# Optimization experiments

Hardware: AMD Instinct MI355X
Metric: run time of the kernel (lower is better)

Reference implementation:

```python
import jax, jax.numpy as jnp
import numpy as np

E = 1024
H = 16
EPS = 1e-5


def setup_inputs() -> dict:
    key = jax.random.key(0)
    ks = jax.random.split(key, 17)
    B, T = 8, 1024
    s = 0.02
    inp = {
        'x': jax.random.normal(ks[0], (B, T, E), dtype=jnp.float32),
        'Wq': jax.random.normal(ks[1], (E, E), dtype=jnp.float32) * s,
        'bq': jnp.zeros((E,), jnp.float32),
        'Wk': jax.random.normal(ks[2], (E, E), dtype=jnp.float32) * s,
        'bk': jnp.zeros((E,), jnp.float32),
        'Wv': jax.random.normal(ks[3], (E, E), dtype=jnp.float32) * s,
        'bv': jnp.zeros((E,), jnp.float32),
        'Wo': jax.random.normal(ks[4], (E, E), dtype=jnp.float32) * s,
        'bo': jnp.zeros((E,), jnp.float32),
        'W1': jax.random.normal(ks[5], (E, 4 * E), dtype=jnp.float32) * s,
        'b1': jnp.zeros((4 * E,), jnp.float32),
        'W2': jax.random.normal(ks[6], (4 * E, E), dtype=jnp.float32) * s,
        'b2': jnp.zeros((E,), jnp.float32),
        'g1': jnp.ones((E,), jnp.float32),
        'be1': jnp.zeros((E,), jnp.float32),
        'g2': jnp.ones((E,), jnp.float32),
        'be2': jnp.zeros((E,), jnp.float32),
    }
    return inp


def _layernorm(x, g, b):
    mu = jnp.mean(x, axis=-1, keepdims=True)
    var = jnp.mean(jnp.square(x - mu), axis=-1, keepdims=True)
    return (x - mu) * jax.lax.rsqrt(var + EPS) * g + b


def _block(x, Wq, bq, Wk, bk, Wv, bv, Wo, bo, W1, b1, W2, b2, g1, be1, g2, be2):
    B, T, Ee = x.shape
    hd = Ee // H
    q = (x @ Wq + bq).reshape(B, T, H, hd).transpose(0, 2, 1, 3)  # (B,H,T,d)
    k = (x @ Wk + bk).reshape(B, T, H, hd).transpose(0, 2, 1, 3)
    v = (x @ Wv + bv).reshape(B, T, H, hd).transpose(0, 2, 1, 3)
    scores = jnp.einsum('bhqd,bhkd->bhqk', q, k) / jnp.sqrt(jnp.float32(hd))
    causal = jnp.tril(jnp.ones((T, T), bool))
    scores = jnp.where(causal, scores, -jnp.inf)
    w = jax.nn.softmax(scores, axis=-1)
    attn = jnp.einsum('bhqk,bhkd->bhqd', w, v)
    attn = attn.transpose(0, 2, 1, 3).reshape(B, T, Ee)
    attn = attn @ Wo + bo  # dropout is identity (p=0 / eval)
    x = _layernorm(x + attn, g1, be1)
    ff = jax.nn.relu(x @ W1 + b1) @ W2 + b2
    x = _layernorm(x + ff, g2, be2)
    return x


def reference(x, Wq, bq, Wk, bk, Wv, bv, Wo, bo, W1, b1, W2, b2, g1, be1, g2, be2):
    return _block(x, Wq, bq, Wk, bk, Wv, bv, Wo, bo, W1, b1, W2, b2, g1, be1, g2, be2)
```

## Files before the change

### kernel.cpp

```cpp
#include <hip/hip_runtime.h>
#include <math.h>

typedef unsigned short u16;
typedef __attribute__((ext_vector_type(8))) short short8;
typedef __attribute__((ext_vector_type(4))) float floatx4;

__device__ __forceinline__ u16 f2bf(float f) {
    unsigned u = __float_as_uint(f);
    unsigned r = u + 0x7fffu + ((u >> 16) & 1u);
    return (u16)(r >> 16);
}

__device__ __forceinline__ void gload16(const u16* g, u16* l) {
    __builtin_amdgcn_global_load_lds((const __attribute__((address_space(1))) void*)g,
                                     (__attribute__((address_space(3))) void*)l, 16, 0, 0);
}

template<int EPI>
__global__ __launch_bounds__(256) void gemm_mfma(
    const u16* __restrict__ A, const u16* __restrict__ Bt,
    const float* __restrict__ bias, const float* __restrict__ bias2,
    const float* __restrict__ bias3, const float* __restrict__ R,
    void* __restrict__ Cout, void* __restrict__ out2, void* __restrict__ out3,
    int M, int N, int K) {
    __shared__ u16 As[128 * 32];
    __shared__ u16 Bs[128 * 32];
    const int tid = threadIdx.x;
    const int wave = tid >> 6, lane = tid & 63;
    const int lrow = lane & 15, quad = lane >> 4;
    const int ny = M >> 7;
    const int by = blockIdx.x % ny, bx = blockIdx.x / ny;
    const int m0 = by * 128, n0 = bx * 128;
    const int wm = (wave & 1) * 64, wn = (wave >> 1) * 64;

    floatx4 acc[4][4];
#pragma unroll
    for (int i = 0; i < 4; i++)
#pragma unroll
        for (int j = 0; j < 4; j++) acc[i][j] = {0.f, 0.f, 0.f, 0.f};

    const int f0 = wave * 128 + lane;

    for (int k0 = 0; k0 < K; k0 += 32) {
        __syncthreads();
#pragma unroll
        for (int i = 0; i < 2; i++) {
            int f = f0 + i * 64;
            int row = f >> 2, c = f & 3;
            int cg = c ^ ((row >> 1) & 3);
            gload16(A + (size_t)(m0 + row) * K + k0 + cg * 8, As + f * 8);
            gload16(Bt + (size_t)(n0 + row) * K + k0 + cg * 8, Bs + f * 8);
        }
        __syncthreads();
        short8 af[4], bf[4];
#pragma unroll
        for (int mt = 0; mt < 4; mt++) {
            int row = wm + mt * 16 + lrow;
            int ch = quad ^ ((lrow >> 1) & 3);
            af[mt] = *(const short8*)(As + row * 32 + ch * 8);
        }
#pragma unroll
        for (int nt = 0; nt < 4; nt++) {
            int row = wn + nt * 16 + lrow;
            int ch = quad ^ ((lrow >> 1) & 3);
            bf[nt] = *(const short8*)(Bs + row * 32 + ch * 8);
        }
#pragma unroll
        for (int mt = 0; mt < 4; mt++)
#pragma unroll
            for (int nt = 0; nt < 4; nt++)
                acc[mt][nt] = __builtin_amdgcn_mfma_f32_16x16x32_bf16(af[mt], bf[nt], acc[mt][nt], 0, 0, 0);
    }

    const float* bp = bias;
    int sec = 0;
    if (EPI == 4) {
        sec = n0 >> 10;
        bp = sec == 0 ? bias : (sec == 1 ? bias2 : bias3);
    }
    float bv[4];
#pragma unroll
    for (int nt = 0; nt < 4; nt++) {
        int gc = n0 + wn + nt * 16 + lrow;
        bv[nt] = bp[EPI == 4 ? (gc & 1023) : gc];
    }

#pragma unroll
    for (int mt = 0; mt < 4; mt++) {
        int gr0 = m0 + wm + mt * 16 + quad * 4;
#pragma unroll
        for (int nt = 0; nt < 4; nt++) {
            int gc = n0 + wn + nt * 16 + lrow;
            floatx4 a = acc[mt][nt];
            if (EPI == 1) {
                u16* C = (u16*)Cout;
#pragma unroll
                for (int r = 0; r < 4; r++)
                    C[(size_t)(gr0 + r) * N + gc] = f2bf(fmaxf(a[r] + bv[nt], 0.f));
            } else if (EPI == 2) {
                float* C = (float*)Cout;
#pragma unroll
                for (int r = 0; r < 4; r++) {
                    size_t idx = (size_t)(gr0 + r) * N + gc;
                    C[idx] = a[r] + bv[nt] + R[idx];
                }
            } else {
                int nc = gc & 1023;
                if (sec < 2) {
                    u16* C = (u16*)(sec == 0 ? Cout : out2);
#pragma unroll
                    for (int r = 0; r < 4; r++)
                        C[(size_t)(gr0 + r) * 1024 + nc] = f2bf(a[r] + bv[nt]);
                } else {
                    u16* C = (u16*)out3;
                    int bb = gr0 >> 10, t0 = gr0 & 1023;
                    size_t idx = ((size_t)(bb * 1024 + nc)) * 1024 + t0;
                    ushort4 u;
                    u.x = f2bf(a[0] + bv[nt]); u.y = f2bf(a[1] + bv[nt]);
                    u.z = f2bf(a[2] + bv[nt]); u.w = f2bf(a[3] + bv[nt]);
                    *(ushort4*)(C + idx) = u;
                }
            }
        }
    }
}

__global__ __launch_bounds__(256) void attn_mfma(
    const u16* __restrict__ q, const u16* __restrict__ k,
    const u16* __restrict__ vT, u16* __restrict__ o) {
    __shared__ u16 Kb[2][64 * 64];
    __shared__ u16 Vb[2][64 * 64];
    __shared__ u16 Pb[4][2][16 * 72];

    const int tid = threadIdx.x;
    const int wave = tid >> 6, lane = tid & 63;
    const int lrow = lane & 15, quad = lane >> 4;
    const int qb = blockIdx.y, bh = blockIdx.x;
    const int b = bh >> 4, h = bh & 15;
    const size_t tokbase = (size_t)b * 1024;
    const int ktmax = qb * 2 + 1;

#pragma unroll
    for (int i = 0; i < 2; i++) {
        int f = wave * 128 + i * 64 + lane;
        int row = f >> 3, c = f & 7, cg = c ^ (row & 7);
        gload16(q + (tokbase + qb * 128 + row) * 1024 + h * 64 + cg * 8, Kb[1] + f * 8);
        gload16(q + (tokbase + qb * 128 + 64 + row) * 1024 + h * 64 + cg * 8, Vb[1] + f * 8);
        gload16(k + (tokbase + row) * 1024 + h * 64 + cg * 8, Kb[0] + f * 8);
        gload16(vT + (tokbase + h * 64 + row) * 1024 + cg * 8, Vb[0] + f * 8);
    }
    asm volatile("s_waitcnt vmcnt(0)" ::: "memory");
    __syncthreads();
    short8 aQ[2][2];
#pragma unroll
    for (int band = 0; band < 2; band++)
#pragma unroll
        for (int ks = 0; ks < 2; ks++) {
            int row = wave * 16 + lrow;
            int pos = (ks * 4 + quad) ^ (lrow & 7);
            const u16* src = band ? Vb[1] : Kb[1];
            aQ[band][ks] = *(const short8*)(src + row * 64 + pos * 8);
        }
    __syncthreads();

    float lp[2][4];
    floatx4 oa[2][4];
#pragma unroll
    for (int bd = 0; bd < 2; bd++)
#pragma unroll
        for (int i = 0; i < 4; i++) { lp[bd][i] = 0.f; oa[bd][i] = {0.f, 0.f, 0.f, 0.f}; }

    for (int kt = 0; kt <= ktmax; kt++) {
        const int cur = kt & 1;
        if (kt < ktmax) {
            const int nxt = cur ^ 1;
#pragma unroll
            for (int i = 0; i < 2; i++) {
                int f = wave * 128 + i * 64 + lane;
                int row = f >> 3, c = f & 7, cg = c ^ (row & 7);
                gload16(k + (tokbase + (kt + 1) * 64 + row) * 1024 + h * 64 + cg * 8, Kb[nxt] + f * 8);
                gload16(vT + (tokbase + h * 64 + row) * 1024 + (kt + 1) * 64 + cg * 8, Vb[nxt] + f * 8);
            }
        }
#pragma unroll
        for (int band = 0; band < 2; band++) {
            const int btile = qb * 2 + band;
            if (kt > btile) continue;
            floatx4 sacc[4];
#pragma unroll
            for (int nt = 0; nt < 4; nt++) sacc[nt] = {0.f, 0.f, 0.f, 0.f};
#pragma unroll
            for (int nt = 0; nt < 4; nt++)
#pragma unroll
                for (int ks = 0; ks < 2; ks++) {
                    int row = nt * 16 + lrow;
                    int pos = (ks * 4 + quad) ^ (lrow & 7);
                    short8 bK = *(const short8*)(Kb[cur] + row * 64 + pos * 8);
                    sacc[nt] = __builtin_amdgcn_mfma_f32_16x16x32_bf16(aQ[band][ks], bK, sacc[nt], 0, 0, 0);
                }
            const bool diag = (kt == btile);
            float p[4][4];
#pragma unroll
            for (int r = 0; r < 4; r++) {
                int qrl = wave * 16 + quad * 4 + r;
#pragma unroll
                for (int nt = 0; nt < 4; nt++) {
                    float e = exp2f(sacc[nt][r] * 0.18033688011112042f);
                    if (diag && (nt * 16 + lrow) > qrl) e = 0.f;
                    p[nt][r] = e;
                    lp[band][r] += e;
                }
            }
            u16* Pw = Pb[wave][band];
#pragma unroll
            for (int nt = 0; nt < 4; nt++)
#pragma unroll
                for (int r = 0; r < 4; r++) {
                    int row = quad * 4 + r, key = nt * 16 + lrow;
                    int pos = ((key >> 3) ^ (row & 7)) * 8 + (key & 7);
                    Pw[row * 72 + pos] = f2bf(p[nt][r]);
                }
            asm volatile("s_waitcnt lgkmcnt(0)" ::: "memory");
            short8 aP[2];
#pragma unroll
            for (int ks = 0; ks < 2; ks++) {
                int pos = (ks * 4 + quad) ^ (lrow & 7);
                aP[ks] = *(const short8*)(Pw + lrow * 72 + pos * 8);
            }
#pragma unroll
            for (int nt = 0; nt < 4; nt++)
#pragma unroll
                for (int ks = 0; ks < 2; ks++) {
                    int row = nt * 16 + lrow;
                    int pos = (ks * 4 + quad) ^ (lrow & 7);
                    short8 bV = *(const short8*)(Vb[cur] + row * 64 + pos * 8);
                    oa[band][nt] = __builtin_amdgcn_mfma_f32_16x16x32_bf16(aP[ks], bV, oa[band][nt], 0, 0, 0);
                }
        }
        __syncthreads();
    }

#pragma unroll
    for (int band = 0; band < 2; band++) {
        float inv[4];
#pragma unroll
        for (int r = 0; r < 4; r++) {
            float l = lp[band][r];
#pragma unroll
            for (int off = 1; off < 16; off <<= 1) l += __shfl_xor(l, off);
            inv[r] = 1.f / l;
        }
#pragma unroll
        for (int nt = 0; nt < 4; nt++)
#pragma unroll
            for (int r = 0; r < 4; r++) {
                int grow = qb * 128 + band * 64 + wave * 16 + quad * 4 + r;
                float v = oa[band][nt][r] * inv[r];
                o[(tokbase + grow) * 1024 + h * 64 + nt * 16 + lrow] = f2bf(v);
            }
    }
}

__device__ __forceinline__ void tconv_tile(const float* __restrict__ W, u16* __restrict__ Wt,
                                           int K, int N, int k0, int n0, int t,
                                           float (*Ts)[33]) {
    const int r = t >> 3, c4 = (t & 7) * 4;
    float4 v = *(const float4*)(W + (size_t)(k0 + r) * N + n0 + c4);
    Ts[c4 + 0][r] = v.x; Ts[c4 + 1][r] = v.y; Ts[c4 + 2][r] = v.z; Ts[c4 + 3][r] = v.w;
    __syncthreads();
    ushort4 u;
    u.x = f2bf(Ts[r][c4 + 0]); u.y = f2bf(Ts[r][c4 + 1]);
    u.z = f2bf(Ts[r][c4 + 2]); u.w = f2bf(Ts[r][c4 + 3]);
    *(ushort4*)(Wt + (size_t)(n0 + r) * K + k0 + c4) = u;
}

__global__ __launch_bounds__(256) void prep_kernel(
    const float* __restrict__ x, const float* __restrict__ Wq, const float* __restrict__ Wk,
    const float* __restrict__ Wv, const float* __restrict__ Wo, const float* __restrict__ W1,
    const float* __restrict__ W2, u16* __restrict__ xb, u16* __restrict__ Wqkvt,
    u16* __restrict__ Wot, u16* __restrict__ W1t, u16* __restrict__ W2t) {
    __shared__ float Ts[32][33];
    const int blk = blockIdx.x, t = threadIdx.x;
    if (blk < 4096) {
        size_t i = ((size_t)blk * 256 + t) * 8;
        float4 a = *(const float4*)(x + i);
        float4 b = *(const float4*)(x + i + 4);
        ushort4 u0, u1;
        u0.x = f2bf(a.x); u0.y = f2bf(a.y); u0.z = f2bf(a.z); u0.w = f2bf(a.w);
        u1.x = f2bf(b.x); u1.y = f2bf(b.y); u1.z = f2bf(b.z); u1.w = f2bf(b.w);
        *(ushort4*)(xb + i) = u0;
        *(ushort4*)(xb + i + 4) = u1;
    } else if (blk < 8192) {
        int s = blk - 4096;
        int which = s >> 10, tt = s & 1023;
        int n0 = (tt & 31) * 32, k0 = (tt >> 5) * 32;
        const float* W = which == 0 ? Wq : which == 1 ? Wk : which == 2 ? Wv : Wo;
        u16* Wt = which == 3 ? Wot : Wqkvt + (size_t)which * 1024 * 1024;
        tconv_tile(W, Wt, 1024, 1024, k0, n0, t, Ts);
    } else if (blk < 12288) {
        int tt = blk - 8192;
        int n0 = (tt & 127) * 32, k0 = (tt >> 7) * 32;
        tconv_tile(W1, W1t, 1024, 4096, k0, n0, t, Ts);
    } else {
        int tt = blk - 12288;
        int n0 = (tt & 31) * 32, k0 = (tt >> 5) * 32;
        tconv_tile(W2, W2t, 4096, 1024, k0, n0, t, Ts);
    }
}

template<int WB>
__global__ __launch_bounds__(256) void ln_kernel(float* __restrict__ x, const float* __restrict__ g,
                                                 const float* __restrict__ bta, u16* __restrict__ xb) {
    __shared__ float red[8];
    const int tid = threadIdx.x;
    float* rowp = x + (size_t)blockIdx.x * 1024;
    float4 val = ((const float4*)rowp)[tid];

    float s = val.x + val.y + val.z + val.w;
#pragma unroll
    for (int off = 32; off; off >>= 1) s += __shfl_down(s, off);
    if ((tid & 63) == 0) red[tid >> 6] = s;
    __syncthreads();
    float mu = (red[0] + red[1] + red[2] + red[3]) * (1.f / 1024.f);

    float dx = val.x - mu, dy = val.y - mu, dz = val.z - mu, dw = val.w - mu;
    float sq = dx * dx + dy * dy + dz * dz + dw * dw;
#pragma unroll
    for (int off = 32; off; off >>= 1) sq += __shfl_down(sq, off);
    if ((tid & 63) == 0) red[4 + (tid >> 6)] = sq;
    __syncthreads();
    float var = (red[4] + red[5] + red[6] + red[7]) * (1.f / 1024.f);
    float rs = rsqrtf(var + 1e-5f);

    float4 gv = ((const float4*)g)[tid];
    float4 bv = ((const float4*)bta)[tid];
    float4 ov;
    ov.x = dx * rs * gv.x + bv.x;
    ov.y = dy * rs * gv.y + bv.y;
    ov.z = dz * rs * gv.z + bv.z;
    ov.w = dw * rs * gv.w + bv.w;
    ((float4*)rowp)[tid] = ov;
    if (WB) {
        u16* rb = xb + (size_t)blockIdx.x * 1024 + tid * 4;
        ushort4 u;
        u.x = f2bf(ov.x); u.y = f2bf(ov.y); u.z = f2bf(ov.z); u.w = f2bf(ov.w);
        *(ushort4*)rb = u;
    }
}

extern "C" void kernel_launch(void* const* d_in, const int* in_sizes, int n_in,
                              void* d_out, int out_size, void* d_ws, size_t ws_size,
                              hipStream_t stream) {
    const float* x   = (const float*)d_in[0];
    const float* Wq  = (const float*)d_in[1];
    const float* bq  = (const float*)d_in[2];
    const float* Wk  = (const float*)d_in[3];
    const float* bk  = (const float*)d_in[4];
    const float* Wv  = (const float*)d_in[5];
    const float* bv  = (const float*)d_in[6];
    const float* Wo  = (const float*)d_in[7];
    const float* bo  = (const float*)d_in[8];
    const float* W1  = (const float*)d_in[9];
    const float* b1  = (const float*)d_in[10];
    const float* W2  = (const float*)d_in[11];
    const float* b2  = (const float*)d_in[12];
    const float* g1  = (const float*)d_in[13];
    const float* be1 = (const float*)d_in[14];
    const float* g2  = (const float*)d_in[15];
    const float* be2 = (const float*)d_in[16];
    float* out = (float*)d_out;

    u16* w = (u16*)d_ws;
    const size_t SZ_ACT = (size_t)8192 * 1024;
    u16* xb    = w;                  w += SZ_ACT;
    u16* Wqkvt = w;                  w += (size_t)3 * 1024 * 1024;
    u16* Wot   = w;                  w += 1024 * 1024;
    u16* W1t   = w;                  w += (size_t)4096 * 1024;
    u16* W2t   = w;                  w += (size_t)1024 * 4096;
    u16* qb    = w;                  w += SZ_ACT;
    u16* kb    = w;                  w += SZ_ACT;
    u16* vTb   = w;                  w += SZ_ACT;
    u16* attb  = w;                  w += SZ_ACT;
    u16* hbuf  = qb;

    const int M = 8192;
    dim3 blk(256);

    prep_kernel<<<dim3(16384), blk, 0, stream>>>(x, Wq, Wk, Wv, Wo, W1, W2,
                                                 xb, Wqkvt, Wot, W1t, W2t);

    gemm_mfma<4><<<dim3(24 * 64), blk, 0, stream>>>(xb, Wqkvt, bq, bk, bv, nullptr,
                                                    qb, kb, vTb, M, 3072, 1024);
    attn_mfma<<<dim3(128, 8), blk, 0, stream>>>(qb, kb, vTb, attb);
    gemm_mfma<2><<<dim3(8 * 64), blk, 0, stream>>>(attb, Wot, bo, nullptr, nullptr, x,
                                                   out, nullptr, nullptr, M, 1024, 1024);
    ln_kernel<1><<<dim3(8192), blk, 0, stream>>>(out, g1, be1, xb);
    gemm_mfma<1><<<dim3(32 * 64), blk, 0, stream>>>(xb, W1t, b1, nullptr, nullptr, nullptr,
                                                    hbuf, nullptr, nullptr, M, 4096, 1024);
    gemm_mfma<2><<<dim3(8 * 64), blk, 0, stream>>>(hbuf, W2t, b2, nullptr, nullptr, out,
                                                   out, nullptr, nullptr, M, 1024, 4096);
    ln_kernel<0><<<dim3(8192), blk, 0, stream>>>(out, g2, be2, nullptr);
}
```

Before: 522.8 us.

## Use 32x32 MFMA tiles and split-K with atomics for the W2 GEMM

Switches the GEMM inner loop from 16x16x32 to 32x32x16 bf16 MFMA instructions, using a 2x2 grid of 32x32 accumulators per wave, which cuts LDS fragment reads per MFMA. Adds a split-K mode for the FFN down-projection (K=4096): it launches twice as many blocks, each covering half of K, and accumulates into the output with float atomics. The residual plus b2 bias is pre-written into the output by the first layernorm kernel so the atomics only add partial sums. This trades higher occupancy on the small-N GEMM for atomic traffic and a summation order that is no longer deterministic.

```diff
diff --git a/kernel.cpp b/kernel.cpp
--- a/kernel.cpp
+++ b/kernel.cpp
@@ -4,6 +4,7 @@
 typedef unsigned short u16;
 typedef __attribute__((ext_vector_type(8))) short short8;
 typedef __attribute__((ext_vector_type(4))) float floatx4;
+typedef __attribute__((ext_vector_type(16))) float floatx16;
 
 __device__ __forceinline__ u16 f2bf(float f) {
     unsigned u = __float_as_uint(f);
@@ -27,21 +28,28 @@
     __shared__ u16 Bs[128 * 32];
     const int tid = threadIdx.x;
     const int wave = tid >> 6, lane = tid & 63;
-    const int lrow = lane & 15, quad = lane >> 4;
-    const int ny = M >> 7;
-    const int by = blockIdx.x % ny, bx = blockIdx.x / ny;
+    const int ar = lane & 31, hl = lane >> 5;
+    const int ny = M >> 7, nx = N >> 7;
+    const int per = ny * nx;
+    const int chunk = blockIdx.x / per, rem = blockIdx.x % per;
+    const int nchunks = gridDim.x / per;
+    const int by = rem % ny, bx = rem / ny;
     const int m0 = by * 128, n0 = bx * 128;
     const int wm = (wave & 1) * 64, wn = (wave >> 1) * 64;
-
-    floatx4 acc[4][4];
-#pragma unroll
-    for (int i = 0; i < 4; i++)
-#pragma unroll
-        for (int j = 0; j < 4; j++) acc[i][j] = {0.f, 0.f, 0.f, 0.f};
+    const int klen = K / nchunks;
+    const int kstart = chunk * klen, kend = kstart + klen;
+
+    floatx16 acc[2][2];
+#pragma unroll
+    for (int i = 0; i < 2; i++)
+#pragma unroll
+        for (int j = 0; j < 2; j++)
+#pragma unroll
+            for (int r = 0; r < 16; r++) acc[i][j][r] = 0.f;
 
     const int f0 = wave * 128 + lane;
 
-    for (int k0 = 0; k0 < K; k0 += 32) {
+    for (int k0 = kstart; k0 < kend; k0 += 32) {
         __syncthreads();
 #pragma unroll
         for (int i = 0; i < 2; i++) {
@@ -52,24 +60,34 @@
             gload16(Bt + (size_t)(n0 + row) * K + k0 + cg * 8, Bs + f * 8);
         }
         __syncthreads();
-        short8 af[4], bf[4];
-#pragma unroll
-        for (int mt = 0; mt < 4; mt++) {
-            int row = wm + mt * 16 + lrow;
-            int ch = quad ^ ((lrow >> 1) & 3);
-            af[mt] = *(const short8*)(As + row * 32 + ch * 8);
-        }
-#pragma unroll
-        for (int nt = 0; nt < 4; nt++) {
-            int row = wn + nt * 16 + lrow;
-            int ch = quad ^ ((lrow >> 1) & 3);
-            bf[nt] = *(const short8*)(Bs + row * 32 + ch * 8);
-        }
-#pragma unroll
-        for (int mt = 0; mt < 4; mt++)
-#pragma unroll
-            for (int nt = 0; nt < 4; nt++)
-                acc[mt][nt] = __builtin_amdgcn_mfma_f32_16x16x32_bf16(af[mt], bf[nt], acc[mt][nt], 0, 0, 0);
+        short8 af[2][2], bf[2][2];
+#pragma unroll
+        for (int mt = 0; mt < 2; mt++) {
+            int row = wm + mt * 32 + ar;
+            int sw = (row >> 1) & 3;
+#pragma unroll
+            for (int s = 0; s < 2; s++) {
+                int ch = (s * 2 + hl) ^ sw;
+                af[mt][s] = *(const short8*)(As + row * 32 + ch * 8);
+            }
+        }
+#pragma unroll
+        for (int nt = 0; nt < 2; nt++) {
+            int row = wn + nt * 32 + ar;
+            int sw = (row >> 1) & 3;
+#pragma unroll
+            for (int s = 0; s < 2; s++) {
+                int ch = (s * 2 + hl) ^ sw;
+                bf[nt][s] = *(const short8*)(Bs + row * 32 + ch * 8);
+            }
+        }
+#pragma unroll
+        for (int s = 0; s < 2; s++)
+#pragma unroll
+            for (int mt = 0; mt < 2; mt++)
+#pragma unroll
+                for (int nt = 0; nt < 2; nt++)
+                    acc[mt][nt] = __builtin_amdgcn_mfma_f32_32x32x16_bf16(af[mt][s], bf[nt][s], acc[mt][nt], 0, 0, 0);
     }
 
     const float* bp = bias;
@@ -78,51 +96,60 @@
         sec = n0 >> 10;
         bp = sec == 0 ? bias : (sec == 1 ? bias2 : bias3);
     }
-    float bv[4];
-#pragma unroll
-    for (int nt = 0; nt < 4; nt++) {
-        int gc = n0 + wn + nt * 16 + lrow;
-        bv[nt] = bp[EPI == 4 ? (gc & 1023) : gc];
-    }
-
-#pragma unroll
-    for (int mt = 0; mt < 4; mt++) {
-        int gr0 = m0 + wm + mt * 16 + quad * 4;
-#pragma unroll
-        for (int nt = 0; nt < 4; nt++) {
-            int gc = n0 + wn + nt * 16 + lrow;
-            floatx4 a = acc[mt][nt];
-            if (EPI == 1) {
-                u16* C = (u16*)Cout;
-#pragma unroll
-                for (int r = 0; r < 4; r++)
-                    C[(size_t)(gr0 + r) * N + gc] = f2bf(fmaxf(a[r] + bv[nt], 0.f));
-            } else if (EPI == 2) {
-                float* C = (float*)Cout;
-#pragma unroll
-                for (int r = 0; r < 4; r++) {
-                    size_t idx = (size_t)(gr0 + r) * N + gc;
-                    C[idx] = a[r] + bv[nt] + R[idx];
+    float bv[2];
+    if (EPI != 5) {
+#pragma unroll
+        for (int nt = 0; nt < 2; nt++) {
+            int gc = n0 + wn + nt * 32 + ar;
+            bv[nt] = bp[EPI == 4 ? (gc & 1023) : gc];
+        }
+    }
+
+#pragma unroll
+    for (int mt = 0; mt < 2; mt++)
+#pragma unroll
+        for (int nt = 0; nt < 2; nt++) {
+            floatx16 a = acc[mt][nt];
+            int gc = n0 + wn + nt * 32 + ar;
+#pragma unroll
+            for (int rg = 0; rg < 4; rg++) {
+                int gr0 = m0 + wm + mt * 32 + rg * 8 + hl * 4;
+                if (EPI == 1) {
+                    u16* C = (u16*)Cout;
+#pragma unroll
+                    for (int rr = 0; rr < 4; rr++)
+                        C[(size_t)(gr0 + rr) * N + gc] = f2bf(fmaxf(a[rg * 4 + rr] + bv[nt], 0.f));
+                } else if (EPI == 2) {
+                    float* C = (float*)Cout;
+#pragma unroll
+                    for (int rr = 0; rr < 4; rr++) {
+                        size_t idx = (size_t)(gr0 + rr) * N + gc;
+                        C[idx] = a[rg * 4 + rr] + bv[nt] + R[idx];
+                    }
+                } else if (EPI == 5) {
+                    float* C = (float*)Cout;
+#pragma unroll
+                    for (int rr = 0; rr < 4; rr++)
+                        unsafeAtomicAdd(&C[(size_t)(gr0 + rr) * N + gc], a[rg * 4 + rr]);
+                } else {
+                    int nc = gc & 1023;
+                    if (sec < 2) {
+                        u16* C = (u16*)(sec == 0 ? Cout : out2);
+#pragma unroll
+                        for (int rr = 0; rr < 4; rr++)
+                            C[(size_t)(gr0 + rr) * 1024 + nc] = f2bf(a[rg * 4 + rr] + bv[nt]);
+                    } else {
+                        u16* C = (u16*)out3;
+                        int bb = gr0 >> 10, t0 = gr0 & 1023;
+                        size_t idx = ((size_t)(bb * 1024 + nc)) * 1024 + t0;
+                        ushort4 u;
+                        u.x = f2bf(a[rg * 4 + 0] + bv[nt]); u.y = f2bf(a[rg * 4 + 1] + bv[nt]);
+                        u.z = f2bf(a[rg * 4 + 2] + bv[nt]); u.w = f2bf(a[rg * 4 + 3] + bv[nt]);
+                        *(ushort4*)(C + idx) = u;
+                    }
                 }
-            } else {
-                int nc = gc & 1023;
-                if (sec < 2) {
-                    u16* C = (u16*)(sec == 0 ? Cout : out2);
-#pragma unroll
-                    for (int r = 0; r < 4; r++)
-                        C[(size_t)(gr0 + r) * 1024 + nc] = f2bf(a[r] + bv[nt]);
-                } else {
-                    u16* C = (u16*)out3;
-                    int bb = gr0 >> 10, t0 = gr0 & 1023;
-                    size_t idx = ((size_t)(bb * 1024 + nc)) * 1024 + t0;
-                    ushort4 u;
-                    u.x = f2bf(a[0] + bv[nt]); u.y = f2bf(a[1] + bv[nt]);
-                    u.z = f2bf(a[2] + bv[nt]); u.w = f2bf(a[3] + bv[nt]);
-                    *(ushort4*)(C + idx) = u;
-                }
-            }
-        }
-    }
+            }
+        }
 }
 
 __global__ __launch_bounds__(256) void attn_mfma(
@@ -308,9 +335,10 @@
     }
 }
 
-template<int WB>
+template<int WB, int ADDB>
 __global__ __launch_bounds__(256) void ln_kernel(float* __restrict__ x, const float* __restrict__ g,
-                                                 const float* __restrict__ bta, u16* __restrict__ xb) {
+                                                 const float* __restrict__ bta, u16* __restrict__ xb,
+                                                 const float* __restrict__ badd) {
     __shared__ float red[8];
     const int tid = threadIdx.x;
     float* rowp = x + (size_t)blockIdx.x * 1024;
@@ -339,13 +367,17 @@
     ov.y = dy * rs * gv.y + bv.y;
     ov.z = dz * rs * gv.z + bv.z;
     ov.w = dw * rs * gv.w + bv.w;
-    ((float4*)rowp)[tid] = ov;
     if (WB) {
         u16* rb = xb + (size_t)blockIdx.x * 1024 + tid * 4;
         ushort4 u;
         u.x = f2bf(ov.x); u.y = f2bf(ov.y); u.z = f2bf(ov.z); u.w = f2bf(ov.w);
         *(ushort4*)rb = u;
     }
+    if (ADDB) {
+        float4 ab = ((const float4*)badd)[tid];
+        ov.x += ab.x; ov.y += ab.y; ov.z += ab.z; ov.w += ab.w;
+    }
+    ((float4*)rowp)[tid] = ov;
 }
 
 extern "C" void kernel_launch(void* const* d_in, const int* in_sizes, int n_in,
@@ -394,10 +426,10 @@
     attn_mfma<<<dim3(128, 8), blk, 0, stream>>>(qb, kb, vTb, attb);
     gemm_mfma<2><<<dim3(8 * 64), blk, 0, stream>>>(attb, Wot, bo, nullptr, nullptr, x,
                                                    out, nullptr, nullptr, M, 1024, 1024);
-    ln_kernel<1><<<dim3(8192), blk, 0, stream>>>(out, g1, be1, xb);
+    ln_kernel<1, 1><<<dim3(8192), blk, 0, stream>>>(out, g1, be1, xb, b2);
     gemm_mfma<1><<<dim3(32 * 64), blk, 0, stream>>>(xb, W1t, b1, nullptr, nullptr, nullptr,
                                                     hbuf, nullptr, nullptr, M, 4096, 1024);
-    gemm_mfma<2><<<dim3(8 * 64), blk, 0, stream>>>(hbuf, W2t, b2, nullptr, nullptr, out,
-                                                   out, nullptr, nullptr, M, 1024, 4096);
-    ln_kernel<0><<<dim3(8192), blk, 0, stream>>>(out, g2, be2, nullptr);
-}
+    gemm_mfma<5><<<dim3(2 * 8 * 64), blk, 0, stream>>>(hbuf, W2t, nullptr, nullptr, nullptr, nullptr,
+                                                       out, nullptr, nullptr, M, 1024, 4096);
+    ln_kernel<0, 0><<<dim3(8192), blk, 0, stream>>>(out, g2, be2, nullptr, nullptr);
+}
```

Result: no change. 527.5 us (+0.9%).
